# Optimization experiments

Hardware: AMD Instinct MI355X
Metric: run time of the kernel (lower is better)

## Reference

```python
import jax, jax.numpy as jnp
import numpy as np

B, S, D_IN, D_OUT = 4, 4096, 1024, 1024

def setup_inputs() -> dict:
    key = jax.random.key(0)
    kx, kq, kk, kv = jax.random.split(key, 4)
    # torch Linear weights are [out, in]; init scale ~ U(-1/sqrt(in), 1/sqrt(in))
    lim = 1.0 / np.sqrt(D_IN)
    x = jax.random.normal(kx, (B, S, D_IN), dtype=jnp.float32)
    W_query = jax.random.uniform(kq, (D_OUT, D_IN), dtype=jnp.float32, minval=-lim, maxval=lim)
    W_key = jax.random.uniform(kk, (D_OUT, D_IN), dtype=jnp.float32, minval=-lim, maxval=lim)
    W_value = jax.random.uniform(kv, (D_OUT, D_IN), dtype=jnp.float32, minval=-lim, maxval=lim)
    return {"x": x, "W_query": W_query, "W_key": W_key, "W_value": W_value}

def reference(x, W_query, W_key, W_value):
    # Linear: x @ W.T  (torch convention, weight shape [out, in])
    q = jnp.einsum('bsd,od->bso', x, W_query)
    k = jnp.einsum('bsd,od->bso', x, W_key)
    v = jnp.einsum('bsd,od->bso', x, W_value)
    scale = 1.0 / jnp.sqrt(jnp.asarray(k.shape[-1], dtype=x.dtype))
    scores = jnp.einsum('bqo,bko->bqk', q, k) * scale  # [B,S,S]
    weights = jax.nn.softmax(scores, axis=-1)
    return jnp.einsum('bqk,bko->bqo', weights, v)  # [B,S,D_OUT]
```

## Files before the change

### kernel.cpp

```cpp
#include <hip/hip_runtime.h>
#include <cstdint>
#include <cstddef>

typedef __attribute__((ext_vector_type(8))) short short8;
typedef __attribute__((ext_vector_type(4))) float f32x4;

__device__ __forceinline__ unsigned short f2bf(float x) {
  union { float f; unsigned u; } v; v.f = x;
  unsigned r = (v.u + 0x7FFFu + ((v.u >> 16) & 1u)) >> 16;
  return (unsigned short)r;
}

#define GLOAD16(g, l)                                                    \
  __builtin_amdgcn_global_load_lds(                                      \
      (const __attribute__((address_space(1))) unsigned int*)(g),        \
      (__attribute__((address_space(3))) unsigned int*)(l), 16, 0, 0)

#define DSR(dst, addrv, imm)                                             \
  asm volatile("ds_read_b128 %0, %1 offset:%c2"                          \
               : "=&v"(dst) : "v"(addrv), "i"(imm))

__global__ __launch_bounds__(256) void cvt_f32_bf16(
    const float* __restrict__ in, unsigned short* __restrict__ out, long n) {
  long i = ((long)blockIdx.x * 256 + threadIdx.x) * 8;
  if (i >= n) return;
  const float4* p = (const float4*)(in + i);
  float4 a = p[0], b = p[1];
  short8 r;
  r[0] = (short)f2bf(a.x); r[1] = (short)f2bf(a.y);
  r[2] = (short)f2bf(a.z); r[3] = (short)f2bf(a.w);
  r[4] = (short)f2bf(b.x); r[5] = (short)f2bf(b.y);
  r[6] = (short)f2bf(b.z); r[7] = (short)f2bf(b.w);
  *(short8*)(out + i) = r;
}

__global__ __launch_bounds__(256) void cvt_w3(
    const float* __restrict__ wa, const float* __restrict__ wb,
    const float* __restrict__ wc, unsigned short* __restrict__ oa,
    unsigned short* __restrict__ ob, unsigned short* __restrict__ oc) {
  int which = blockIdx.x >> 9;
  long i = ((long)(blockIdx.x & 511) * 256 + threadIdx.x) * 8;
  const float* in = which == 0 ? wa : which == 1 ? wb : wc;
  unsigned short* out = which == 0 ? oa : which == 1 ? ob : oc;
  const float4* p = (const float4*)(in + i);
  float4 a = p[0], b = p[1];
  short8 r;
  r[0] = (short)f2bf(a.x); r[1] = (short)f2bf(a.y);
  r[2] = (short)f2bf(a.z); r[3] = (short)f2bf(a.w);
  r[4] = (short)f2bf(b.x); r[5] = (short)f2bf(b.y);
  r[6] = (short)f2bf(b.z); r[7] = (short)f2bf(b.w);
  *(short8*)(out + i) = r;
}

__global__ __launch_bounds__(256) void reduce_rsum(
    const float* __restrict__ part, float* __restrict__ outr,
    size_t stride, int n) {
  int i = blockIdx.x * 256 + threadIdx.x;
  if (i >= n) return;
  float s = 0.f;
#pragma unroll
  for (int p = 0; p < 64; p++) s += part[(size_t)p * stride + i];
  outr[i] = 1.0f / s;
}

template <int MODE>
__global__ __launch_bounds__(512, 2) void gemm_bt256(
    const unsigned short* __restrict__ A, int lda, size_t asb,
    const unsigned short* __restrict__ B, int ldb, size_t bsb,
    void* __restrict__ C, int ldc, size_t csb,
    float* __restrict__ rs, int rss, size_t rsp,
    int nbn, int K, float scale) {
  __shared__ unsigned short As[2][256 * 64];
  __shared__ unsigned short Bs[2][256 * 64];

  A += (size_t)blockIdx.y * asb;
  B += (size_t)blockIdx.y * bsb;
  char* Cb = (char*)C + (size_t)blockIdx.y * csb * (MODE == 3 ? 4 : 2);
  rs += (size_t)blockIdx.y * rss;

  unsigned bid = blockIdx.x;
  unsigned cpx = gridDim.x >> 3;
  unsigned swz = (bid & 7u) * cpx + (bid >> 3);
  int bm = (int)(swz / (unsigned)nbn);
  int bn = (int)(swz % (unsigned)nbn);
  int m0 = bm * 256, n0 = bn * 256;

  int t512 = threadIdx.x;
  int lane = t512 & 63, wid = t512 >> 6;
  int wm = wid >> 2, wn = wid & 3;
  int l15 = lane & 15, l4 = lane >> 4;

  int srow = t512 >> 3;
  int g = (t512 & 7) ^ ((t512 >> 3) & 7);
  const unsigned short* pa = A + (size_t)(m0 + srow) * lda + g * 8;
  const unsigned short* pb = B + (size_t)(n0 + srow) * ldb + g * 8;

  f32x4 acc[8][4] = {};

  const int NT = K >> 6;

#define STAGE(jj, buf)                                                    \
  do {                                                                    \
    int _k0 = (jj) << 6;                                                  \
    _Pragma("unroll") for (int i = 0; i < 4; i++)                         \
        GLOAD16(pa + (size_t)(i * 64) * lda + _k0,                        \
                (char*)As[buf] + i * 8192 + t512 * 16);                   \
    _Pragma("unroll") for (int i = 0; i < 4; i++)                         \
        GLOAD16(pb + (size_t)(i * 64) * ldb + _k0,                        \
                (char*)Bs[buf] + i * 8192 + t512 * 16);                   \
  } while (0)

  unsigned c0 = ((unsigned)l4) ^ (unsigned)(l15 & 7);
  unsigned c1 = (4u | (unsigned)l4) ^ (unsigned)(l15 & 7);
  unsigned rowA = (unsigned)(wm * 128 + l15) * 128u;
  unsigned rowB = (unsigned)(wn * 64 + l15) * 128u;

  STAGE(0, 0);

  for (int j = 0; j < NT; ++j) {
    int cur = j & 1;
    __builtin_amdgcn_sched_barrier(0);
    __builtin_amdgcn_s_barrier();
    if (j + 1 < NT) {
      STAGE(j + 1, cur ^ 1);
      asm volatile("s_waitcnt vmcnt(8)" ::: "memory");
    } else {
      asm volatile("s_waitcnt vmcnt(0)" ::: "memory");
    }
    __builtin_amdgcn_s_barrier();

    unsigned baseA = (unsigned)(uintptr_t)(
        (__attribute__((address_space(3))) char*)(&As[cur][0]));
    unsigned baseB = (unsigned)(uintptr_t)(
        (__attribute__((address_space(3))) char*)(&Bs[cur][0]));
    unsigned aA0 = baseA + rowA + c0 * 16, aA1 = baseA + rowA + c1 * 16;
    unsigned aB0 = baseB + rowB + c0 * 16, aB1 = baseB + rowB + c1 * 16;

    short8 afq[2][2][2];
    short8 bfv[4][2];

    DSR(afq[0][0][0], aA0, 0);
    DSR(afq[0][0][1], aA1, 0);
    DSR(afq[0][1][0], aA0, 2048);
    DSR(afq[0][1][1], aA1, 2048);
#pragma unroll
    for (int ni = 0; ni < 4; ni++) {
      DSR(bfv[ni][0], aB0, ni * 2048);
      DSR(bfv[ni][1], aB1, ni * 2048);
    }

#pragma unroll
    for (int p = 0; p < 4; ++p) {
      if (p < 3) {
        const int mi0 = (p + 1) * 2;
        DSR(afq[(p + 1) & 1][0][0], aA0, mi0 * 2048);
        DSR(afq[(p + 1) & 1][0][1], aA1, mi0 * 2048);
        DSR(afq[(p + 1) & 1][1][0], aA0, (mi0 + 1) * 2048);
        DSR(afq[(p + 1) & 1][1][1], aA1, (mi0 + 1) * 2048);
        asm volatile("s_waitcnt lgkmcnt(4)" ::: "memory");
      } else {
        asm volatile("s_waitcnt lgkmcnt(0)" ::: "memory");
      }
      __builtin_amdgcn_sched_barrier(0);
      __builtin_amdgcn_s_setprio(1);
#pragma unroll
      for (int ks = 0; ks < 2; ks++)
#pragma unroll
        for (int m2 = 0; m2 < 2; m2++) {
          int mi = p * 2 + m2;
#pragma unroll
          for (int ni = 0; ni < 4; ni++)
            acc[mi][ni] = __builtin_amdgcn_mfma_f32_16x16x32_bf16(
                afq[p & 1][m2][ks], bfv[ni][ks], acc[mi][ni], 0, 0, 0);
        }
      __builtin_amdgcn_s_setprio(0);
      __builtin_amdgcn_sched_barrier(0);
    }
  }
#undef STAGE

  if constexpr (MODE == 2) {
    float sums[8][4];
#pragma unroll
    for (int mi = 0; mi < 8; mi++)
#pragma unroll
      for (int jj = 0; jj < 4; jj++) sums[mi][jj] = 0.f;
#pragma unroll
    for (int mi = 0; mi < 8; mi++)
#pragma unroll
      for (int ni = 0; ni < 4; ni++)
#pragma unroll
        for (int jj = 0; jj < 4; jj++) {
          int row = m0 + wm * 128 + mi * 16 + l4 * 4 + jj;
          int col = n0 + wn * 64 + ni * 16 + l15;
          float e = __expf(acc[mi][ni][jj] * scale);
          sums[mi][jj] += e;
          ((unsigned short*)Cb)[(size_t)row * ldc + col] = f2bf(e);
        }
    size_t pslot = (size_t)(bn * 4 + wn) * rsp;
#pragma unroll
    for (int mi = 0; mi < 8; mi++)
#pragma unroll
      for (int jj = 0; jj < 4; jj++) {
        float s = sums[mi][jj];
        s += __shfl_xor(s, 1);
        s += __shfl_xor(s, 2);
        s += __shfl_xor(s, 4);
        s += __shfl_xor(s, 8);
        if (l15 == 0) {
          int row = m0 + wm * 128 + mi * 16 + l4 * 4 + jj;
          rs[pslot + row] = s;
        }
      }
  } else {
#pragma unroll
    for (int mi = 0; mi < 8; mi++) {
      float inv[4];
      if constexpr (MODE == 3) {
#pragma unroll
        for (int jj = 0; jj < 4; jj++) {
          int row = m0 + wm * 128 + mi * 16 + l4 * 4 + jj;
          inv[jj] = rs[row];
        }
      }
#pragma unroll
      for (int ni = 0; ni < 4; ni++)
#pragma unroll
        for (int jj = 0; jj < 4; jj++) {
          int row = m0 + wm * 128 + mi * 16 + l4 * 4 + jj;
          int col = n0 + wn * 64 + ni * 16 + l15;
          float val = acc[mi][ni][jj];
          if constexpr (MODE == 1)
            ((unsigned short*)Cb)[(size_t)row * ldc + col] = f2bf(val * scale);
          else
            ((float*)Cb)[(size_t)row * ldc + col] = val * inv[jj];
        }
    }
  }
}

extern "C" void kernel_launch(void* const* d_in, const int* in_sizes, int n_in,
                              void* d_out, int out_size, void* d_ws, size_t ws_size,
                              hipStream_t stream) {
  (void)in_sizes; (void)n_in; (void)out_size;
  const float* x  = (const float*)d_in[0];
  const float* Wq = (const float*)d_in[1];
  const float* Wk = (const float*)d_in[2];
  const float* Wv = (const float*)d_in[3];
  float* out = (float*)d_out;

  const int Bn = 4, S = 4096, D = 1024;
  const size_t MS = (size_t)Bn * S;
  const float scale = 0.03125f;

  char* ws = (char*)d_ws;
  unsigned short* QKb = (unsigned short*)ws; ws += MS * 2048 * 2;
  unsigned short* VTb = (unsigned short*)ws; ws += MS * D * 2;
  unsigned short* Sreg = (unsigned short*)ws;
  const size_t s4_bytes = (size_t)Bn * S * S * 2;
  const size_t s1_bytes = (size_t)S * S * 2;
  size_t head = (size_t)(ws - (char*)d_ws);
  bool batched = ws_size >= head + s4_bytes + 16u * 1024 * 1024;
  ws += batched ? s4_bytes : s1_bytes;
  unsigned short* wqkb = (unsigned short*)ws; ws += (size_t)2048 * D * 2;
  unsigned short* wvb  = (unsigned short*)ws; ws += (size_t)D * D * 2;
  float* rpart = (float*)ws; ws += 64 * MS * sizeof(float);
  float* rinv  = (float*)ws;
  unsigned short* xb = Sreg;

  cvt_f32_bf16<<<8192, 256, 0, stream>>>(x, xb, (long)MS * D);
  cvt_w3<<<1536, 256, 0, stream>>>(Wq, Wk, Wv, wqkb, wqkb + (size_t)D * D, wvb);

  gemm_bt256<1><<<dim3(512, 1), 512, 0, stream>>>(
      xb, D, 0, wqkb, D, 0, QKb, 2048, 0, nullptr, 0, 0, 8, D, 1.0f);
  gemm_bt256<1><<<dim3(256, 1), 512, 0, stream>>>(
      wvb, D, 0, xb, D, 0, VTb, (int)MS, 0, nullptr, 0, 0, 64, D, 1.0f);

  if (batched) {
    gemm_bt256<2><<<dim3(256, Bn), 512, 0, stream>>>(
        QKb, 2048, (size_t)S * 2048,
        QKb + 1024, 2048, (size_t)S * 2048,
        Sreg, S, (size_t)S * S, rpart, S, MS, 16, D, scale);
    reduce_rsum<<<(int)(MS / 256), 256, 0, stream>>>(rpart, rinv, MS, (int)MS);
    gemm_bt256<3><<<dim3(64, Bn), 512, 0, stream>>>(
        Sreg, S, (size_t)S * S,
        VTb, (int)MS, (size_t)S,
        out, D, (size_t)S * D, rinv, S, 0, 4, S, 1.0f);
  } else {
    for (int b = 0; b < Bn; b++) {
      const unsigned short* Qx = QKb + (size_t)b * S * 2048;
      const unsigned short* Kx = Qx + 1024;
      gemm_bt256<2><<<dim3(256, 1), 512, 0, stream>>>(
          Qx, 2048, 0, Kx, 2048, 0, Sreg, S, 0,
          rpart + (size_t)b * S, 0, MS, 16, D, scale);
      reduce_rsum<<<S / 256, 256, 0, stream>>>(
          rpart + (size_t)b * S, rinv + (size_t)b * S, MS, S);
      gemm_bt256<3><<<dim3(64, 1), 512, 0, stream>>>(
          Sreg, S, 0, VTb + (size_t)b * S, (int)MS, 0,
          out + (size_t)b * S * D, D, 0, rinv + (size_t)b * S, 0, 0,
          4, S, 1.0f);
    }
  }
}
```

Measured before the change: 418.7 us.

## Switch GEMM inner loop to 32x32x16 MFMA with plain LDS loads

Replaces the 16x16x32 bf16 MFMA tiling with 32x32x16 MFMA tiles (4x2 accumulators of 16 floats per wave). The hand-scheduled inline-asm ds_read pipeline, with its lgkmcnt waits, setprio and sched_barrier, is dropped in favour of plain compiler-generated LDS loads that fetch all fragments before the MFMAs. The epilogues for all three modes are rewritten for the 32x32 output layout. The larger MFMA needs fewer instructions and fewer LDS reads per FLOP, but the compiler may schedule it worse than the manual overlap of LDS reads with MFMAs.

New measurement: 469.6 us. 1.12x slower.

```diff
diff --git a/kernel.cpp b/kernel.cpp
--- a/kernel.cpp
+++ b/kernel.cpp
@@ -3,7 +3,7 @@
 #include <cstddef>
 
 typedef __attribute__((ext_vector_type(8))) short short8;
-typedef __attribute__((ext_vector_type(4))) float f32x4;
+typedef __attribute__((ext_vector_type(16))) float f32x16;
 
 __device__ __forceinline__ unsigned short f2bf(float x) {
   union { float f; unsigned u; } v; v.f = x;
@@ -15,10 +15,6 @@
   __builtin_amdgcn_global_load_lds(                                      \
       (const __attribute__((address_space(1))) unsigned int*)(g),        \
       (__attribute__((address_space(3))) unsigned int*)(l), 16, 0, 0)
-
-#define DSR(dst, addrv, imm)                                             \
-  asm volatile("ds_read_b128 %0, %1 offset:%c2"                          \
-               : "=&v"(dst) : "v"(addrv), "i"(imm))
 
 __global__ __launch_bounds__(256) void cvt_f32_bf16(
     const float* __restrict__ in, unsigned short* __restrict__ out, long n) {
@@ -88,14 +84,14 @@
   int t512 = threadIdx.x;
   int lane = t512 & 63, wid = t512 >> 6;
   int wm = wid >> 2, wn = wid & 3;
-  int l15 = lane & 15, l4 = lane >> 4;
+  int l31 = lane & 31, l5 = lane >> 5;
 
   int srow = t512 >> 3;
   int g = (t512 & 7) ^ ((t512 >> 3) & 7);
   const unsigned short* pa = A + (size_t)(m0 + srow) * lda + g * 8;
   const unsigned short* pb = B + (size_t)(n0 + srow) * ldb + g * 8;
 
-  f32x4 acc[8][4] = {};
+  f32x16 acc[4][2] = {};
 
   const int NT = K >> 6;
 
@@ -110,11 +106,6 @@
                 (char*)Bs[buf] + i * 8192 + t512 * 16);                   \
   } while (0)
 
-  unsigned c0 = ((unsigned)l4) ^ (unsigned)(l15 & 7);
-  unsigned c1 = (4u | (unsigned)l4) ^ (unsigned)(l15 & 7);
-  unsigned rowA = (unsigned)(wm * 128 + l15) * 128u;
-  unsigned rowB = (unsigned)(wn * 64 + l15) * 128u;
-
   STAGE(0, 0);
 
   for (int j = 0; j < NT; ++j) {
@@ -129,112 +120,89 @@
     }
     __builtin_amdgcn_s_barrier();
 
-    unsigned baseA = (unsigned)(uintptr_t)(
-        (__attribute__((address_space(3))) char*)(&As[cur][0]));
-    unsigned baseB = (unsigned)(uintptr_t)(
-        (__attribute__((address_space(3))) char*)(&Bs[cur][0]));
-    unsigned aA0 = baseA + rowA + c0 * 16, aA1 = baseA + rowA + c1 * 16;
-    unsigned aB0 = baseB + rowB + c0 * 16, aB1 = baseB + rowB + c1 * 16;
-
-    short8 afq[2][2][2];
-    short8 bfv[4][2];
-
-    DSR(afq[0][0][0], aA0, 0);
-    DSR(afq[0][0][1], aA1, 0);
-    DSR(afq[0][1][0], aA0, 2048);
-    DSR(afq[0][1][1], aA1, 2048);
-#pragma unroll
-    for (int ni = 0; ni < 4; ni++) {
-      DSR(bfv[ni][0], aB0, ni * 2048);
-      DSR(bfv[ni][1], aB1, ni * 2048);
-    }
-
-#pragma unroll
-    for (int p = 0; p < 4; ++p) {
-      if (p < 3) {
-        const int mi0 = (p + 1) * 2;
-        DSR(afq[(p + 1) & 1][0][0], aA0, mi0 * 2048);
-        DSR(afq[(p + 1) & 1][0][1], aA1, mi0 * 2048);
-        DSR(afq[(p + 1) & 1][1][0], aA0, (mi0 + 1) * 2048);
-        DSR(afq[(p + 1) & 1][1][1], aA1, (mi0 + 1) * 2048);
-        asm volatile("s_waitcnt lgkmcnt(4)" ::: "memory");
-      } else {
-        asm volatile("s_waitcnt lgkmcnt(0)" ::: "memory");
-      }
-      __builtin_amdgcn_sched_barrier(0);
-      __builtin_amdgcn_s_setprio(1);
-#pragma unroll
-      for (int ks = 0; ks < 2; ks++)
-#pragma unroll
-        for (int m2 = 0; m2 < 2; m2++) {
-          int mi = p * 2 + m2;
-#pragma unroll
-          for (int ni = 0; ni < 4; ni++)
-            acc[mi][ni] = __builtin_amdgcn_mfma_f32_16x16x32_bf16(
-                afq[p & 1][m2][ks], bfv[ni][ks], acc[mi][ni], 0, 0, 0);
-        }
-      __builtin_amdgcn_s_setprio(0);
-      __builtin_amdgcn_sched_barrier(0);
-    }
+    const char* Ab = (const char*)As[cur];
+    const char* Bb = (const char*)Bs[cur];
+
+    short8 bfv[2][4], afv[4][4];
+#pragma unroll
+    for (int nt = 0; nt < 2; nt++)
+#pragma unroll
+      for (int ks = 0; ks < 4; ks++) {
+        int r = wn * 64 + nt * 32 + l31;
+        int c = (ks * 2 + l5) ^ (r & 7);
+        bfv[nt][ks] = *(const short8*)(Bb + r * 128 + c * 16);
+      }
+#pragma unroll
+    for (int mt = 0; mt < 4; mt++)
+#pragma unroll
+      for (int ks = 0; ks < 4; ks++) {
+        int r = wm * 128 + mt * 32 + l31;
+        int c = (ks * 2 + l5) ^ (r & 7);
+        afv[mt][ks] = *(const short8*)(Ab + r * 128 + c * 16);
+      }
+#pragma unroll
+    for (int ks = 0; ks < 4; ks++)
+#pragma unroll
+      for (int mt = 0; mt < 4; mt++)
+#pragma unroll
+        for (int nt = 0; nt < 2; nt++)
+          acc[mt][nt] = __builtin_amdgcn_mfma_f32_32x32x16_bf16(
+              afv[mt][ks], bfv[nt][ks], acc[mt][nt], 0, 0, 0);
   }
 #undef STAGE
 
   if constexpr (MODE == 2) {
-    float sums[8][4];
-#pragma unroll
-    for (int mi = 0; mi < 8; mi++)
-#pragma unroll
-      for (int jj = 0; jj < 4; jj++) sums[mi][jj] = 0.f;
-#pragma unroll
-    for (int mi = 0; mi < 8; mi++)
-#pragma unroll
-      for (int ni = 0; ni < 4; ni++)
-#pragma unroll
-        for (int jj = 0; jj < 4; jj++) {
-          int row = m0 + wm * 128 + mi * 16 + l4 * 4 + jj;
-          int col = n0 + wn * 64 + ni * 16 + l15;
-          float e = __expf(acc[mi][ni][jj] * scale);
-          sums[mi][jj] += e;
-          ((unsigned short*)Cb)[(size_t)row * ldc + col] = f2bf(e);
-        }
     size_t pslot = (size_t)(bn * 4 + wn) * rsp;
 #pragma unroll
-    for (int mi = 0; mi < 8; mi++)
-#pragma unroll
-      for (int jj = 0; jj < 4; jj++) {
-        float s = sums[mi][jj];
+    for (int mt = 0; mt < 4; mt++) {
+      float sums16[16];
+#pragma unroll
+      for (int reg = 0; reg < 16; reg++) {
+        int row = m0 + wm * 128 + mt * 32 + (reg & 3) + 8 * (reg >> 2) + 4 * l5;
+        float e0 = __expf(acc[mt][0][reg] * scale);
+        float e1 = __expf(acc[mt][1][reg] * scale);
+        ((unsigned short*)Cb)[(size_t)row * ldc + n0 + wn * 64 + l31] = f2bf(e0);
+        ((unsigned short*)Cb)[(size_t)row * ldc + n0 + wn * 64 + 32 + l31] =
+            f2bf(e1);
+        sums16[reg] = e0 + e1;
+      }
+#pragma unroll
+      for (int reg = 0; reg < 16; reg++) {
+        float s = sums16[reg];
         s += __shfl_xor(s, 1);
         s += __shfl_xor(s, 2);
         s += __shfl_xor(s, 4);
         s += __shfl_xor(s, 8);
-        if (l15 == 0) {
-          int row = m0 + wm * 128 + mi * 16 + l4 * 4 + jj;
+        s += __shfl_xor(s, 16);
+        if (l31 == 0) {
+          int row =
+              m0 + wm * 128 + mt * 32 + (reg & 3) + 8 * (reg >> 2) + 4 * l5;
           rs[pslot + row] = s;
         }
       }
+    }
   } else {
 #pragma unroll
-    for (int mi = 0; mi < 8; mi++) {
-      float inv[4];
-      if constexpr (MODE == 3) {
-#pragma unroll
-        for (int jj = 0; jj < 4; jj++) {
-          int row = m0 + wm * 128 + mi * 16 + l4 * 4 + jj;
-          inv[jj] = rs[row];
+    for (int mt = 0; mt < 4; mt++) {
+#pragma unroll
+      for (int reg = 0; reg < 16; reg++) {
+        int row = m0 + wm * 128 + mt * 32 + (reg & 3) + 8 * (reg >> 2) + 4 * l5;
+        if constexpr (MODE == 1) {
+#pragma unroll
+          for (int nt = 0; nt < 2; nt++) {
+            int col = n0 + wn * 64 + nt * 32 + l31;
+            ((unsigned short*)Cb)[(size_t)row * ldc + col] =
+                f2bf(acc[mt][nt][reg] * scale);
+          }
+        } else {
+          float iv = rs[row];
+#pragma unroll
+          for (int nt = 0; nt < 2; nt++) {
+            int col = n0 + wn * 64 + nt * 32 + l31;
+            ((float*)Cb)[(size_t)row * ldc + col] = acc[mt][nt][reg] * iv;
+          }
         }
       }
-#pragma unroll
-      for (int ni = 0; ni < 4; ni++)
-#pragma unroll
-        for (int jj = 0; jj < 4; jj++) {
-          int row = m0 + wm * 128 + mi * 16 + l4 * 4 + jj;
-          int col = n0 + wn * 64 + ni * 16 + l15;
-          float val = acc[mi][ni][jj];
-          if constexpr (MODE == 1)
-            ((unsigned short*)Cb)[(size_t)row * ldc + col] = f2bf(val * scale);
-          else
-            ((float*)Cb)[(size_t)row * ldc + col] = val * inv[jj];
-        }
     }
   }
 }
```

## Fold Wq and Wk into one matrix so scores use x·M·xᵀ

Applied to the files above, without the earlier changes.

The change precomputes M = Wqᵀ·Wk (via transposed bf16 copies and a small 128-tile GEMM). It then computes xM = x·M once and forms the scores as xM·xᵀ. This replaces the 2048-wide Q/K projection with a 1024-wide one plus a tiny 1024³ GEMM, cutting projection FLOPs roughly in half. The cost is an extra bf16 rounding of M before it is applied, and x now needs its own buffer instead of being aliased into the score region.

Result: faster. 406.8 us (-2.8%).

```diff
diff --git a/kernel.cpp b/kernel.cpp
--- a/kernel.cpp
+++ b/kernel.cpp
@@ -34,22 +34,29 @@
   *(short8*)(out + i) = r;
 }
 
-__global__ __launch_bounds__(256) void cvt_w3(
-    const float* __restrict__ wa, const float* __restrict__ wb,
-    const float* __restrict__ wc, unsigned short* __restrict__ oa,
-    unsigned short* __restrict__ ob, unsigned short* __restrict__ oc) {
-  int which = blockIdx.x >> 9;
-  long i = ((long)(blockIdx.x & 511) * 256 + threadIdx.x) * 8;
-  const float* in = which == 0 ? wa : which == 1 ? wb : wc;
-  unsigned short* out = which == 0 ? oa : which == 1 ? ob : oc;
-  const float4* p = (const float4*)(in + i);
-  float4 a = p[0], b = p[1];
-  short8 r;
-  r[0] = (short)f2bf(a.x); r[1] = (short)f2bf(a.y);
-  r[2] = (short)f2bf(a.z); r[3] = (short)f2bf(a.w);
-  r[4] = (short)f2bf(b.x); r[5] = (short)f2bf(b.y);
-  r[6] = (short)f2bf(b.z); r[7] = (short)f2bf(b.w);
-  *(short8*)(out + i) = r;
+__global__ __launch_bounds__(256) void transpose_cvt2(
+    const float* __restrict__ wq, const float* __restrict__ wk,
+    unsigned short* __restrict__ oq, unsigned short* __restrict__ ok) {
+  __shared__ float tile[64][65];
+  int b = blockIdx.x;
+  const float* in = (b & 256) ? wk : wq;
+  unsigned short* out = (b & 256) ? ok : oq;
+  int tb = b & 255;
+  int O0 = (tb >> 4) * 64;
+  int I0 = (tb & 15) * 64;
+  int t = threadIdx.x;
+  int r0 = t >> 6, c = t & 63;
+#pragma unroll
+  for (int r = 0; r < 16; r++) {
+    int row = r * 4 + r0;
+    tile[row][c] = in[(size_t)(O0 + row) * 1024 + I0 + c];
+  }
+  __syncthreads();
+#pragma unroll
+  for (int r = 0; r < 16; r++) {
+    int irow = r * 4 + r0;
+    out[(size_t)(I0 + irow) * 1024 + O0 + c] = f2bf(tile[c][irow]);
+  }
 }
 
 __global__ __launch_bounds__(256) void reduce_rsum(
@@ -61,6 +68,79 @@
 #pragma unroll
   for (int p = 0; p < 64; p++) s += part[(size_t)p * stride + i];
   outr[i] = 1.0f / s;
+}
+
+__global__ __launch_bounds__(256) void gemm128(
+    const unsigned short* __restrict__ A, int lda,
+    const unsigned short* __restrict__ B, int ldb,
+    unsigned short* __restrict__ C, int ldc,
+    int nbn, int K, float scale) {
+  __shared__ unsigned short As[128 * 64];
+  __shared__ unsigned short Bs[128 * 64];
+
+  unsigned bid = blockIdx.x;
+  unsigned cpx = gridDim.x >> 3;
+  unsigned swz = (bid & 7u) * cpx + (bid >> 3);
+  int bm = (int)(swz / (unsigned)nbn);
+  int bn = (int)(swz % (unsigned)nbn);
+  int m0 = bm * 128, n0 = bn * 128;
+
+  int t = threadIdx.x;
+  int lane = t & 63, wid = t >> 6;
+  int wm = wid >> 1, wn = wid & 1;
+  int l15 = lane & 15, l4 = lane >> 4;
+
+  int srow = t >> 3;
+  int g = (t & 7) ^ ((t >> 3) & 7);
+  const unsigned short* pa = A + (size_t)(m0 + srow) * lda + g * 8;
+  const unsigned short* pb = B + (size_t)(n0 + srow) * ldb + g * 8;
+
+  f32x4 acc[4][4] = {};
+
+  for (int k0 = 0; k0 < K; k0 += 64) {
+    __syncthreads();
+#pragma unroll
+    for (int i = 0; i < 4; i++) {
+      GLOAD16(pa + (size_t)(32 * i) * lda + k0,
+              (char*)As + (size_t)(i * 256 + wid * 64) * 16);
+      GLOAD16(pb + (size_t)(32 * i) * ldb + k0,
+              (char*)Bs + (size_t)(i * 256 + wid * 64) * 16);
+    }
+    __syncthreads();
+#pragma unroll
+    for (int ks = 0; ks < 2; ks++) {
+      short8 af[4], bfr[4];
+#pragma unroll
+      for (int mi = 0; mi < 4; mi++) {
+        int r = wm * 64 + mi * 16 + l15;
+        int c = ((ks << 2) | l4) ^ (r & 7);
+        af[mi] = *(const short8*)((const char*)As + r * 128 + c * 16);
+      }
+#pragma unroll
+      for (int ni = 0; ni < 4; ni++) {
+        int r = wn * 64 + ni * 16 + l15;
+        int c = ((ks << 2) | l4) ^ (r & 7);
+        bfr[ni] = *(const short8*)((const char*)Bs + r * 128 + c * 16);
+      }
+#pragma unroll
+      for (int mi = 0; mi < 4; mi++)
+#pragma unroll
+        for (int ni = 0; ni < 4; ni++)
+          acc[mi][ni] = __builtin_amdgcn_mfma_f32_16x16x32_bf16(
+              af[mi], bfr[ni], acc[mi][ni], 0, 0, 0);
+    }
+  }
+
+#pragma unroll
+  for (int mi = 0; mi < 4; mi++)
+#pragma unroll
+    for (int ni = 0; ni < 4; ni++)
+#pragma unroll
+      for (int j = 0; j < 4; j++) {
+        int row = m0 + wm * 64 + mi * 16 + l4 * 4 + j;
+        int col = n0 + wn * 64 + ni * 16 + l15;
+        C[(size_t)row * ldc + col] = f2bf(acc[mi][ni][j] * scale);
+      }
 }
 
 template <int MODE>
@@ -254,7 +334,8 @@
   const float scale = 0.03125f;
 
   char* ws = (char*)d_ws;
-  unsigned short* QKb = (unsigned short*)ws; ws += MS * 2048 * 2;
+  unsigned short* xb  = (unsigned short*)ws; ws += MS * D * 2;
+  unsigned short* xMb = (unsigned short*)ws; ws += MS * D * 2;
   unsigned short* VTb = (unsigned short*)ws; ws += MS * D * 2;
   unsigned short* Sreg = (unsigned short*)ws;
   const size_t s4_bytes = (size_t)Bn * S * S * 2;
@@ -262,24 +343,29 @@
   size_t head = (size_t)(ws - (char*)d_ws);
   bool batched = ws_size >= head + s4_bytes + 16u * 1024 * 1024;
   ws += batched ? s4_bytes : s1_bytes;
-  unsigned short* wqkb = (unsigned short*)ws; ws += (size_t)2048 * D * 2;
-  unsigned short* wvb  = (unsigned short*)ws; ws += (size_t)D * D * 2;
+  unsigned short* wqT = (unsigned short*)ws; ws += (size_t)D * D * 2;
+  unsigned short* wkT = (unsigned short*)ws; ws += (size_t)D * D * 2;
+  unsigned short* MTb = (unsigned short*)ws; ws += (size_t)D * D * 2;
+  unsigned short* wvb = (unsigned short*)ws; ws += (size_t)D * D * 2;
   float* rpart = (float*)ws; ws += 64 * MS * sizeof(float);
   float* rinv  = (float*)ws;
-  unsigned short* xb = Sreg;
 
   cvt_f32_bf16<<<8192, 256, 0, stream>>>(x, xb, (long)MS * D);
-  cvt_w3<<<1536, 256, 0, stream>>>(Wq, Wk, Wv, wqkb, wqkb + (size_t)D * D, wvb);
-
-  gemm_bt256<1><<<dim3(512, 1), 512, 0, stream>>>(
-      xb, D, 0, wqkb, D, 0, QKb, 2048, 0, nullptr, 0, 0, 8, D, 1.0f);
+  cvt_f32_bf16<<<512, 256, 0, stream>>>(Wv, wvb, (long)D * D);
+  transpose_cvt2<<<512, 256, 0, stream>>>(Wq, Wk, wqT, wkT);
+
+  gemm128<<<64, 256, 0, stream>>>(wkT, D, wqT, D, MTb, D, 8, D, 1.0f);
+
   gemm_bt256<1><<<dim3(256, 1), 512, 0, stream>>>(
       wvb, D, 0, xb, D, 0, VTb, (int)MS, 0, nullptr, 0, 0, 64, D, 1.0f);
 
+  gemm_bt256<1><<<dim3(256, 1), 512, 0, stream>>>(
+      xb, D, 0, MTb, D, 0, xMb, D, 0, nullptr, 0, 0, 4, D, 1.0f);
+
   if (batched) {
     gemm_bt256<2><<<dim3(256, Bn), 512, 0, stream>>>(
-        QKb, 2048, (size_t)S * 2048,
-        QKb + 1024, 2048, (size_t)S * 2048,
+        xMb, D, (size_t)S * D,
+        xb, D, (size_t)S * D,
         Sreg, S, (size_t)S * S, rpart, S, MS, 16, D, scale);
     reduce_rsum<<<(int)(MS / 256), 256, 0, stream>>>(rpart, rinv, MS, (int)MS);
     gemm_bt256<3><<<dim3(64, Bn), 512, 0, stream>>>(
@@ -288,11 +374,10 @@
         out, D, (size_t)S * D, rinv, S, 0, 4, S, 1.0f);
   } else {
     for (int b = 0; b < Bn; b++) {
-      const unsigned short* Qx = QKb + (size_t)b * S * 2048;
-      const unsigned short* Kx = Qx + 1024;
       gemm_bt256<2><<<dim3(256, 1), 512, 0, stream>>>(
-          Qx, 2048, 0, Kx, 2048, 0, Sreg, S, 0,
-          rpart + (size_t)b * S, 0, MS, 16, D, scale);
+          xMb + (size_t)b * S * D, D, 0,
+          xb + (size_t)b * S * D, D, 0,
+          Sreg, S, 0, rpart + (size_t)b * S, 0, MS, 16, D, scale);
       reduce_rsum<<<S / 256, 256, 0, stream>>>(
           rpart + (size_t)b * S, rinv + (size_t)b * S, MS, S);
       gemm_bt256<3><<<dim3(64, 1), 512, 0, stream>>>(
```
